# Kernel optimization log

Hardware: AMD Instinct MI355X
Metric: run time of the kernel (lower is better)

The kernel has to match this reference:

```python
import jax, jax.numpy as jnp
import numpy as np

B, CIN, H, W = 128, 64, 32, 32
COUT, K, STRIDE, PAD = 64, 3, 1, 1
HO = (H + 2 * PAD - K) // STRIDE + 1
WO = (W + 2 * PAD - K) // STRIDE + 1


def setup_inputs() -> dict:
    key = jax.random.key(0)
    k1, k2 = jax.random.split(key)
    x = jax.random.normal(k1, (B, CIN, H, W), dtype=jnp.float32)
    # weight scaled like torch init: randn / sqrt(k*k*Cin) (orthogonal_ in torch just
    # re-orthogonalizes; scale here matches the fan-in normalization)
    weight = jax.random.normal(k2, (HO, WO, COUT, CIN, K, K), dtype=jnp.float32) / np.sqrt(K * K * CIN)
    bias = jnp.full((COUT, HO, WO), 0.5, dtype=jnp.float32)
    return {"x": x, "weight": weight, "bias": bias}


def reference(x, weight, bias):
    # pad spatial dims
    xp = jnp.pad(x, ((0, 0), (0, 0), (PAD, PAD), (PAD, PAD)))
    # gather row windows: [B, C, Ho, K, Wp]
    ri = (jnp.arange(HO) * STRIDE)[:, None] + jnp.arange(K)[None, :]  # [Ho, K]
    ci = (jnp.arange(WO) * STRIDE)[:, None] + jnp.arange(K)[None, :]  # [Wo, K]
    rows = xp[:, :, ri, :]           # [B, C, Ho, K, Wp]
    patches = rows[:, :, :, :, ci]   # [B, C, Ho, K, Wo, K]
    # per-location matmul: b c h p w q , h w d c p q -> b d h w
    out = jnp.einsum('bchpwq,hwdcpq->bdhw', patches, weight)
    return out + bias[None]
```

## Files before the change

### kernel.cpp

```cpp
#include <hip/hip_runtime.h>
#include <hip/hip_bf16.h>

#define KT 576

typedef __attribute__((ext_vector_type(8))) short  short8;
typedef __attribute__((ext_vector_type(4))) float  f32x4;

#define VMCNT(n) asm volatile("s_waitcnt vmcnt(" #n ")" ::: "memory")
#define SB() __builtin_amdgcn_sched_barrier(0)

__device__ __forceinline__ unsigned short f2bf(float f) {
  union { float f; unsigned int u; } v; v.f = f;
  return (unsigned short)((v.u + 0x7FFFu + ((v.u >> 16) & 1u)) >> 16);
}

__global__ __launch_bounds__(256) void xC2_kernel(const float* __restrict__ x,
                                                  unsigned short* __restrict__ xC2) {
  const int hp = blockIdx.x, bb = blockIdx.y, t = threadIdx.x;
  __shared__ unsigned short tile[32 * 1024];
  const bool interior = (hp >= 1 && hp <= 32);
  if (interior) {
#pragma unroll 4
    for (int i = 0; i < 32; ++i) {
      const int row = i * 32 + (t >> 3);
      const int bl = row >> 6, c = row & 63;
      const int k = t & 7;
      const float4 v = *(const float4*)(x + ((size_t)(bb * 16 + bl) * 64 + c) * 1024 +
                                        (hp - 1) * 32 + k * 4);
      const int base = (k * 4) * 1024 + (c >> 3) * 128 + bl * 8 + (c & 7);
      tile[base]        = f2bf(v.x);
      tile[base + 1024] = f2bf(v.y);
      tile[base + 2048] = f2bf(v.z);
      tile[base + 3072] = f2bf(v.w);
    }
  }
  __syncthreads();
  unsigned short* dst = xC2 + (size_t)hp * 278528 + (size_t)bb * 1024;
  const uint4 z = make_uint4(0u, 0u, 0u, 0u);
  for (int idx = t; idx < 34 * 128; idx += 256) {
    const int wp = idx >> 7, s = idx & 127;
    uint4 v = z;
    if (interior && wp >= 1 && wp <= 32) v = *(const uint4*)&tile[(wp - 1) * 1024 + s * 8];
    *(uint4*)(dst + (size_t)wp * 8192 + s * 8) = v;
  }
}

__global__ __launch_bounds__(256, 1) void lc_main(const float* __restrict__ Wt,
                                                  const float* __restrict__ bias,
                                                  const unsigned short* __restrict__ xC2,
                                                  float* __restrict__ out) {
  __shared__ unsigned short Wl[2][32 * KT];
  __shared__ float blds[128];

  const int bid = (int)blockIdx.x;
  const int swz = (bid & 7) * 64 + (bid >> 3);
  const int h = swz >> 4, rem = swz & 15, wq = rem >> 1, half = rem & 1;
  const int t = threadIdx.x, lane = t & 63, wv = t >> 6;
  const int l15 = lane & 15, lg = lane >> 4;

  if (t < 128)
    blds[t] = bias[(half * 32 + (t & 31)) * 1024 + h * 32 + wq * 4 + (t >> 5)];

  const unsigned short* xA = xC2 + (size_t)wv * 2048 + lg * 128 + l15 * 8;
  const int x7 = l15 & 7;
  const int wrow0 = l15 * KT;
  const int wrow1 = (16 + l15) * KT;

  f32x4 acc[4][2][2];
#pragma unroll
  for (int j = 0; j < 4; ++j)
#pragma unroll
    for (int bt = 0; bt < 2; ++bt)
#pragma unroll
      for (int dt = 0; dt < 2; ++dt) acc[j][bt][dt] = (f32x4){0.f, 0.f, 0.f, 0.f};

  short8 As0[3][3], As1[3][3];
  float4 wreg[6];

#define ISSUE_W6(jj, bb)                                                      \
  {                                                                           \
    const float* ws = Wt + (size_t)(h * 32 + wq * 4 + (jj)) * (64 * KT) +     \
                      (size_t)half * (32 * KT);                               \
    _Pragma("unroll")                                                         \
    for (int i = 0; i < 6; ++i) {                                             \
      const float4* p = (const float4*)ws + (((bb) * 6 + i) * 256 + t);       \
      asm volatile("global_load_dwordx4 %0, %1, off" : "=v"(wreg[i]) : "v"(p)); \
    }                                                                         \
  }

#define ISSUE_A(K)                                                            \
  {                                                                           \
    _Pragma("unroll")                                                         \
    for (int s = 0; s < 3; ++s) {                                             \
      const int step = ((K) % 6) * 3 + s;                                     \
      const int pq = step >> 1, p = pq / 3, q = pq - p * 3;                   \
      const size_t off = (size_t)(h + p) * 278528 +                           \
                         (size_t)(wq * 4 + (K) / 6 + q) * 8192 + (step & 1) * 512; \
      const short8* p0 = (const short8*)(xA + off);                           \
      const short8* p1 = (const short8*)(xA + off + 1024);                    \
      asm volatile("global_load_dwordx4 %0, %1, off" : "=v"(As0[(K) % 3][s]) : "v"(p0)); \
      asm volatile("global_load_dwordx4 %0, %1, off" : "=v"(As1[(K) % 3][s]) : "v"(p1)); \
    }                                                                         \
  }

#define SCATTER6(buf, bb)                                                     \
  {                                                                           \
    _Pragma("unroll")                                                         \
    for (int i = 0; i < 6; ++i) {                                             \
      const int f = ((((bb) * 6) + i) * 256 + t) * 4;                         \
      const int d = (((unsigned)(f >> 6)) * 7282u) >> 16;                     \
      int kn = f - d * 576;                                                   \
      int c = ((unsigned)kn * 7282u) >> 16;                                   \
      int r = kn - c * 9;                                                     \
      const float vv[4] = {wreg[i].x, wreg[i].y, wreg[i].z, wreg[i].w};       \
      _Pragma("unroll")                                                       \
      for (int jx = 0; jx < 4; ++jx) {                                        \
        const int kp = r * 64 + c;                                            \
        const int sigma = ((c >> 3) * 9 + r);                                 \
        const int slot = sigma ^ (d & 7);                                     \
        Wl[buf][d * KT + slot * 8 + (kp & 7)] = f2bf(vv[jx]);                 \
        if (++r == 9) { r = 0; ++c; }                                         \
      }                                                                       \
    }                                                                         \
  }

#define MFMAS(jj, gg)                                                         \
  {                                                                           \
    _Pragma("unroll")                                                         \
    for (int s = 0; s < 3; ++s) {                                             \
      const int sb = ((gg) * 3 + s) * 4 + lg;                                 \
      const int sg = (sb & 7) * 9 + (sb >> 3);                                \
      const short8 b0 = *(const short8*)&Wl[(jj) & 1][wrow0 + ((sg ^ x7) << 3)]; \
      const short8 b1 = *(const short8*)&Wl[(jj) & 1][wrow1 + ((sg ^ x7) << 3)]; \
      acc[(jj)][0][0] = __builtin_amdgcn_mfma_f32_16x16x32_bf16(As0[((jj) * 6 + (gg)) % 3][s], b0, acc[(jj)][0][0], 0, 0, 0); \
      acc[(jj)][1][0] = __builtin_amdgcn_mfma_f32_16x16x32_bf16(As1[((jj) * 6 + (gg)) % 3][s], b0, acc[(jj)][1][0], 0, 0, 0); \
      acc[(jj)][0][1] = __builtin_amdgcn_mfma_f32_16x16x32_bf16(As0[((jj) * 6 + (gg)) % 3][s], b1, acc[(jj)][0][1], 0, 0, 0); \
      acc[(jj)][1][1] = __builtin_amdgcn_mfma_f32_16x16x32_bf16(As1[((jj) * 6 + (gg)) % 3][s], b1, acc[(jj)][1][1], 0, 0, 0); \
    }                                                                         \
  }

#define STEP(jj, gg, NN) { VMCNT(NN); SB(); MFMAS(jj, gg) }

#define PHASE(jj)                                                             \
  STEP(jj, 0, 12); ISSUE_A(6 * (jj) + 3); ISSUE_W6((jj) + 1, 0);              \
  STEP(jj, 1, 18); ISSUE_A(6 * (jj) + 4);                                     \
  STEP(jj, 2, 18); ISSUE_A(6 * (jj) + 5);                                     \
    VMCNT(12); SB(); SCATTER6(((jj) + 1) & 1, 0); ISSUE_W6((jj) + 1, 1);      \
  STEP(jj, 3, 18); ISSUE_A(6 * (jj) + 6);                                     \
  STEP(jj, 4, 18); ISSUE_A(6 * (jj) + 7);                                     \
    VMCNT(12); SB(); SCATTER6(((jj) + 1) & 1, 1); ISSUE_W6((jj) + 1, 2);      \
  STEP(jj, 5, 18); ISSUE_A(6 * (jj) + 8);                                     \
    VMCNT(6); SB(); SCATTER6(((jj) + 1) & 1, 2);                              \
  __syncthreads(); SB();

  ISSUE_W6(0, 0); ISSUE_A(0);
  VMCNT(6); SB(); SCATTER6(0, 0); ISSUE_W6(0, 1); ISSUE_A(1);
  VMCNT(6); SB(); SCATTER6(0, 1); ISSUE_W6(0, 2); ISSUE_A(2);
  VMCNT(6); SB(); SCATTER6(0, 2);
  __syncthreads(); SB();

  PHASE(0)
  PHASE(1)
  PHASE(2)

  STEP(3, 0, 12); ISSUE_A(21);
  STEP(3, 1, 12); ISSUE_A(22);
  STEP(3, 2, 12); ISSUE_A(23);
  STEP(3, 3, 12);
  STEP(3, 4, 6);
  STEP(3, 5, 0);

#pragma unroll
  for (int dt = 0; dt < 2; ++dt) {
    const int dd = dt * 16 + l15;
    const int dg = half * 32 + dd;
    const float bv0 = blds[dd], bv1 = blds[32 + dd], bv2 = blds[64 + dd], bv3 = blds[96 + dd];
#pragma unroll
    for (int bt = 0; bt < 2; ++bt) {
#pragma unroll
      for (int i = 0; i < 4; ++i) {
        const int b = wv * 32 + bt * 16 + lg * 4 + i;
        float4 v;
        v.x = acc[0][bt][dt][i] + bv0;
        v.y = acc[1][bt][dt][i] + bv1;
        v.z = acc[2][bt][dt][i] + bv2;
        v.w = acc[3][bt][dt][i] + bv3;
        *(float4*)(out + (size_t)b * 65536 + (size_t)dg * 1024 + h * 32 + wq * 4) = v;
      }
    }
  }
}

extern "C" void kernel_launch(void* const* d_in, const int* in_sizes, int n_in,
                              void* d_out, int out_size, void* d_ws, size_t ws_size,
                              hipStream_t stream) {
  const float* x    = (const float*)d_in[0];
  const float* wt   = (const float*)d_in[1];
  const float* bias = (const float*)d_in[2];
  float* out        = (float*)d_out;
  unsigned short* xC2 = (unsigned short*)d_ws;

  xC2_kernel<<<dim3(34, 8), 256, 0, stream>>>(x, xC2);
  lc_main<<<512, 256, 0, stream>>>(wt, bias, xC2, out);
}
```

Before: 62.26 us.

## Split output channels into quarters per block and double grid size

Each block now computes 16 output channels instead of 32, halving LDS weight buffers, weight register staging and accumulators, and launching 1024 blocks instead of 512. The intent is to raise occupancy and parallelism so the weight stream is better latency-hidden. The cost is that every block reloads the same activation tiles, doubling activation traffic, and the MFMA work per loaded A fragment halves. The vmcnt wait counts are retuned for the smaller per-stage load batches.

```diff
diff --git a/kernel.cpp b/kernel.cpp
--- a/kernel.cpp
+++ b/kernel.cpp
@@ -49,41 +49,38 @@
                                                   const float* __restrict__ bias,
                                                   const unsigned short* __restrict__ xC2,
                                                   float* __restrict__ out) {
-  __shared__ unsigned short Wl[2][32 * KT];
-  __shared__ float blds[128];
+  __shared__ unsigned short Wl[2][16 * KT];
+  __shared__ float blds[64];
 
   const int bid = (int)blockIdx.x;
-  const int swz = (bid & 7) * 64 + (bid >> 3);
-  const int h = swz >> 4, rem = swz & 15, wq = rem >> 1, half = rem & 1;
+  const int swz = (bid & 7) * 128 + (bid >> 3);
+  const int quad = swz & 3, wq = (swz >> 2) & 7, h = swz >> 5;
   const int t = threadIdx.x, lane = t & 63, wv = t >> 6;
   const int l15 = lane & 15, lg = lane >> 4;
 
-  if (t < 128)
-    blds[t] = bias[(half * 32 + (t & 31)) * 1024 + h * 32 + wq * 4 + (t >> 5)];
+  if (t < 64)
+    blds[t] = bias[(quad * 16 + (t & 15)) * 1024 + h * 32 + wq * 4 + (t >> 4)];
 
   const unsigned short* xA = xC2 + (size_t)wv * 2048 + lg * 128 + l15 * 8;
   const int x7 = l15 & 7;
-  const int wrow0 = l15 * KT;
-  const int wrow1 = (16 + l15) * KT;
+  const int wrow = l15 * KT;
 
-  f32x4 acc[4][2][2];
+  f32x4 acc[4][2];
 #pragma unroll
   for (int j = 0; j < 4; ++j)
 #pragma unroll
-    for (int bt = 0; bt < 2; ++bt)
-#pragma unroll
-      for (int dt = 0; dt < 2; ++dt) acc[j][bt][dt] = (f32x4){0.f, 0.f, 0.f, 0.f};
+    for (int bt = 0; bt < 2; ++bt) acc[j][bt] = (f32x4){0.f, 0.f, 0.f, 0.f};
 
   short8 As0[3][3], As1[3][3];
-  float4 wreg[6];
+  float4 wreg[3];
 
-#define ISSUE_W6(jj, bb)                                                      \
+#define ISSUE_W3(jj, bb)                                                      \
   {                                                                           \
     const float* ws = Wt + (size_t)(h * 32 + wq * 4 + (jj)) * (64 * KT) +     \
-                      (size_t)half * (32 * KT);                               \
+                      (size_t)quad * (16 * KT);                               \
     _Pragma("unroll")                                                         \
-    for (int i = 0; i < 6; ++i) {                                             \
-      const float4* p = (const float4*)ws + (((bb) * 6 + i) * 256 + t);       \
+    for (int i = 0; i < 3; ++i) {                                             \
+      const float4* p = (const float4*)ws + (((bb) * 3 + i) * 256 + t);       \
       asm volatile("global_load_dwordx4 %0, %1, off" : "=v"(wreg[i]) : "v"(p)); \
     }                                                                         \
   }
@@ -103,11 +100,11 @@
     }                                                                         \
   }
 
-#define SCATTER6(buf, bb)                                                     \
+#define SCATTER3(buf, bb)                                                     \
   {                                                                           \
     _Pragma("unroll")                                                         \
-    for (int i = 0; i < 6; ++i) {                                             \
-      const int f = ((((bb) * 6) + i) * 256 + t) * 4;                         \
+    for (int i = 0; i < 3; ++i) {                                             \
+      const int f = ((((bb) * 3) + i) * 256 + t) * 4;                         \
       const int d = (((unsigned)(f >> 6)) * 7282u) >> 16;                     \
       int kn = f - d * 576;                                                   \
       int c = ((unsigned)kn * 7282u) >> 16;                                   \
@@ -130,61 +127,58 @@
     for (int s = 0; s < 3; ++s) {                                             \
       const int sb = ((gg) * 3 + s) * 4 + lg;                                 \
       const int sg = (sb & 7) * 9 + (sb >> 3);                                \
-      const short8 b0 = *(const short8*)&Wl[(jj) & 1][wrow0 + ((sg ^ x7) << 3)]; \
-      const short8 b1 = *(const short8*)&Wl[(jj) & 1][wrow1 + ((sg ^ x7) << 3)]; \
-      acc[(jj)][0][0] = __builtin_amdgcn_mfma_f32_16x16x32_bf16(As0[((jj) * 6 + (gg)) % 3][s], b0, acc[(jj)][0][0], 0, 0, 0); \
-      acc[(jj)][1][0] = __builtin_amdgcn_mfma_f32_16x16x32_bf16(As1[((jj) * 6 + (gg)) % 3][s], b0, acc[(jj)][1][0], 0, 0, 0); \
-      acc[(jj)][0][1] = __builtin_amdgcn_mfma_f32_16x16x32_bf16(As0[((jj) * 6 + (gg)) % 3][s], b1, acc[(jj)][0][1], 0, 0, 0); \
-      acc[(jj)][1][1] = __builtin_amdgcn_mfma_f32_16x16x32_bf16(As1[((jj) * 6 + (gg)) % 3][s], b1, acc[(jj)][1][1], 0, 0, 0); \
+      const short8 b0 = *(const short8*)&Wl[(jj) & 1][wrow + ((sg ^ x7) << 3)]; \
+      acc[(jj)][0] = __builtin_amdgcn_mfma_f32_16x16x32_bf16(As0[((jj) * 6 + (gg)) % 3][s], b0, acc[(jj)][0], 0, 0, 0); \
+      acc[(jj)][1] = __builtin_amdgcn_mfma_f32_16x16x32_bf16(As1[((jj) * 6 + (gg)) % 3][s], b0, acc[(jj)][1], 0, 0, 0); \
     }                                                                         \
   }
 
 #define STEP(jj, gg, NN) { VMCNT(NN); SB(); MFMAS(jj, gg) }
+#define STEPNW(jj, gg)   { SB(); MFMAS(jj, gg) }
 
 #define PHASE(jj)                                                             \
-  STEP(jj, 0, 12); ISSUE_A(6 * (jj) + 3); ISSUE_W6((jj) + 1, 0);              \
-  STEP(jj, 1, 18); ISSUE_A(6 * (jj) + 4);                                     \
-  STEP(jj, 2, 18); ISSUE_A(6 * (jj) + 5);                                     \
-    VMCNT(12); SB(); SCATTER6(((jj) + 1) & 1, 0); ISSUE_W6((jj) + 1, 1);      \
-  STEP(jj, 3, 18); ISSUE_A(6 * (jj) + 6);                                     \
-  STEP(jj, 4, 18); ISSUE_A(6 * (jj) + 7);                                     \
-    VMCNT(12); SB(); SCATTER6(((jj) + 1) & 1, 1); ISSUE_W6((jj) + 1, 2);      \
-  STEP(jj, 5, 18); ISSUE_A(6 * (jj) + 8);                                     \
-    VMCNT(6); SB(); SCATTER6(((jj) + 1) & 1, 2);                              \
+  STEPNW(jj, 0);   ISSUE_A(6 * (jj) + 3); ISSUE_W3((jj) + 1, 0);              \
+  STEPNW(jj, 1);   ISSUE_A(6 * (jj) + 4);                                     \
+  STEP(jj, 2, 15); ISSUE_A(6 * (jj) + 5);                                     \
+    VMCNT(12); SB(); SCATTER3(((jj) + 1) & 1, 0); ISSUE_W3((jj) + 1, 1);      \
+  STEPNW(jj, 3);   ISSUE_A(6 * (jj) + 6);                                     \
+  STEP(jj, 4, 15); ISSUE_A(6 * (jj) + 7);                                     \
+    VMCNT(12); SB(); SCATTER3(((jj) + 1) & 1, 1); ISSUE_W3((jj) + 1, 2);      \
+  STEPNW(jj, 5);   ISSUE_A(6 * (jj) + 8);                                     \
+    VMCNT(6); SB(); SCATTER3(((jj) + 1) & 1, 2);                              \
   __syncthreads(); SB();
 
-  ISSUE_W6(0, 0); ISSUE_A(0);
-  VMCNT(6); SB(); SCATTER6(0, 0); ISSUE_W6(0, 1); ISSUE_A(1);
-  VMCNT(6); SB(); SCATTER6(0, 1); ISSUE_W6(0, 2); ISSUE_A(2);
-  VMCNT(6); SB(); SCATTER6(0, 2);
+  ISSUE_W3(0, 0); ISSUE_A(0);
+  VMCNT(6); SB(); SCATTER3(0, 0); ISSUE_W3(0, 1); ISSUE_A(1);
+  VMCNT(6); SB(); SCATTER3(0, 1); ISSUE_W3(0, 2); ISSUE_A(2);
+  VMCNT(6); SB(); SCATTER3(0, 2);
   __syncthreads(); SB();
 
   PHASE(0)
   PHASE(1)
   PHASE(2)
 
-  STEP(3, 0, 12); ISSUE_A(21);
-  STEP(3, 1, 12); ISSUE_A(22);
+  STEPNW(3, 0);   ISSUE_A(21);
+  STEPNW(3, 1);   ISSUE_A(22);
   STEP(3, 2, 12); ISSUE_A(23);
   STEP(3, 3, 12);
   STEP(3, 4, 6);
   STEP(3, 5, 0);
 
-#pragma unroll
-  for (int dt = 0; dt < 2; ++dt) {
-    const int dd = dt * 16 + l15;
-    const int dg = half * 32 + dd;
-    const float bv0 = blds[dd], bv1 = blds[32 + dd], bv2 = blds[64 + dd], bv3 = blds[96 + dd];
+  {
+    const int dg = quad * 16 + l15;
+    const float bv0 = blds[l15], bv1 = blds[16 + l15],
+                bv2 = blds[32 + l15], bv3 = blds[48 + l15];
 #pragma unroll
     for (int bt = 0; bt < 2; ++bt) {
 #pragma unroll
       for (int i = 0; i < 4; ++i) {
         const int b = wv * 32 + bt * 16 + lg * 4 + i;
         float4 v;
-        v.x = acc[0][bt][dt][i] + bv0;
-        v.y = acc[1][bt][dt][i] + bv1;
-        v.z = acc[2][bt][dt][i] + bv2;
-        v.w = acc[3][bt][dt][i] + bv3;
+        v.x = acc[0][bt][i] + bv0;
+        v.y = acc[1][bt][i] + bv1;
+        v.z = acc[2][bt][i] + bv2;
+        v.w = acc[3][bt][i] + bv3;
         *(float4*)(out + (size_t)b * 65536 + (size_t)dg * 1024 + h * 32 + wq * 4) = v;
       }
     }
@@ -201,5 +195,5 @@
   unsigned short* xC2 = (unsigned short*)d_ws;
 
   xC2_kernel<<<dim3(34, 8), 256, 0, stream>>>(x, xC2);
-  lc_main<<<512, 256, 0, stream>>>(wt, bias, xC2, out);
+  lc_main<<<1024, 256, 0, stream>>>(wt, bias, xC2, out);
 }
```

After: 63.08 us. About the same (+1.3%).
